# Optimization experiments

Measured on AMD Instinct MI355X. Metric: run time of the kernel, lower is better.

Reference implementation:

```python
import jax, jax.numpy as jnp
import numpy as np

N_NODES = 245760      # 8192 graphs * 30 atoms
N_GRAPHS = 8192
N_EDGES = 1000000
NODES_PER_GRAPH = 30
F_NODE = 78
F_CELL = 1000
HID = 64


def _lin(key, fan_in, fan_out):
    kw, kb = jax.random.split(key)
    s = 1.0 / np.sqrt(fan_in)
    W = jax.random.uniform(kw, (fan_in, fan_out), minval=-s, maxval=s, dtype=jnp.float32)
    b = jax.random.uniform(kb, (fan_out,), minval=-s, maxval=s, dtype=jnp.float32)
    return W, b


def setup_inputs() -> dict:
    key = jax.random.key(0)
    ks = jax.random.split(key, 14)
    x = jax.random.normal(ks[0], (N_NODES, F_NODE), dtype=jnp.float32)
    # edges constrained within each graph: node = graph_id * 30 + local offset
    offs = jax.random.randint(ks[1], (2, N_EDGES), 0, NODES_PER_GRAPH)
    ge = jax.random.randint(ks[2], (N_EDGES,), 0, N_GRAPHS)
    edge_index = (ge[None, :] * NODES_PER_GRAPH + offs).astype(jnp.int64)
    batch = jnp.repeat(jnp.arange(N_GRAPHS, dtype=jnp.int64), NODES_PER_GRAPH)
    cell_features = jax.random.normal(ks[3], (N_GRAPHS, F_CELL), dtype=jnp.float32)
    W1, b1 = _lin(ks[4], F_NODE, HID)
    W2, b2 = _lin(ks[5], HID, 2 * HID)
    W3, b3 = _lin(ks[6], 2 * HID, 4 * HID)
    Wd, bd = _lin(ks[7], 4 * HID, HID)          # drug_embed_fc
    Wc1, bc1 = _lin(ks[8], F_CELL, 2 * HID)      # cell_fc1
    Wc2, bc2 = _lin(ks[9], 2 * HID, HID)         # cell_fc2
    Wm1, bm1 = _lin(ks[10], 2 * HID, HID)        # combiner_fc1
    Wm2, bm2 = _lin(ks[11], HID, 32)             # combiner_fc2
    Wo, bo = _lin(ks[12], 32, 1)                 # output_fc
    return {"x": x, "edge_index": edge_index, "batch": batch,
            "cell_features": cell_features,
            "W1": W1, "b1": b1, "W2": W2, "b2": b2, "W3": W3, "b3": b3,
            "Wd": Wd, "bd": bd, "Wc1": Wc1, "bc1": bc1, "Wc2": Wc2, "bc2": bc2,
            "Wm1": Wm1, "bm1": bm1, "Wm2": Wm2, "bm2": bm2, "Wo": Wo, "bo": bo}


def _gcn_conv(h, W, b, srcA, dstA, norm, n_nodes):
    # PyG GCNConv: linear transform, then sym-normalized scatter-add (self-loops included in srcA/dstA/norm)
    h = h @ W                                   # [N, out]
    msg = h[srcA] * norm[:, None]               # gather + edge scaling
    out = jnp.zeros((n_nodes, W.shape[1]), h.dtype).at[dstA].add(msg)
    return out + b


def reference(x, edge_index, batch, cell_features,
              W1, b1, W2, b2, W3, b3, Wd, bd,
              Wc1, bc1, Wc2, bc2, Wm1, bm1, Wm2, bm2, Wo, bo):
    n = x.shape[0]
    loops = jnp.arange(n, dtype=edge_index.dtype)
    srcA = jnp.concatenate([edge_index[0], loops])
    dstA = jnp.concatenate([edge_index[1], loops])
    deg = jax.ops.segment_sum(jnp.ones_like(dstA, dtype=x.dtype), dstA, num_segments=n)
    dinv = jax.lax.rsqrt(deg)                   # deg >= 1 due to self-loops
    norm = dinv[srcA] * dinv[dstA]

    h = jax.nn.relu(_gcn_conv(x, W1, b1, srcA, dstA, norm, n))
    h = jax.nn.relu(_gcn_conv(h, W2, b2, srcA, dstA, norm, n))
    h = jax.nn.relu(_gcn_conv(h, W3, b3, srcA, dstA, norm, n))

    # global mean pool over graphs
    sums = jax.ops.segment_sum(h, batch, num_segments=N_GRAPHS)
    cnts = jax.ops.segment_sum(jnp.ones((n,), h.dtype), batch, num_segments=N_GRAPHS)
    drug = (sums / cnts[:, None]) @ Wd + bd     # [B, HID]

    cell = jax.nn.relu(cell_features @ Wc1 + bc1)
    cell = cell @ Wc2 + bc2                      # [B, HID]

    comb = jnp.concatenate([drug, cell], axis=1)
    z = jax.nn.relu(comb @ Wm1 + bm1)
    z = jax.nn.relu(z @ Wm2 + bm2)
    out = z @ Wo + bo
    return out.reshape(-1)
```

## Files before the change

### kernel.cpp

```cpp
#include <hip/hip_runtime.h>

typedef __attribute__((ext_vector_type(8))) short short8;
typedef __attribute__((ext_vector_type(4))) short short4v;
typedef __attribute__((ext_vector_type(4))) float f32x4;
typedef unsigned short u16;

__device__ __forceinline__ u16 f2bf(float f) {
    union { float f; unsigned u; } v; v.f = f;
    unsigned r = v.u + 0x7FFFu + ((v.u >> 16) & 1u);
    return (u16)(r >> 16);
}
__device__ __forceinline__ float bf2f(u16 h) {
    union { unsigned u; float f; } v; v.u = ((unsigned)h) << 16;
    return v.f;
}
__device__ __forceinline__ void split2(float f, u16& h, u16& l) {
    h = f2bf(f);
    l = f2bf(f - bf2f(h));
}
__device__ __forceinline__ short8 ld8(const u16* p) {
    short4v a = *(const short4v*)p;
    short4v b = *(const short4v*)(p + 4);
    short8 r;
    r[0] = a[0]; r[1] = a[1]; r[2] = a[2]; r[3] = a[3];
    r[4] = b[0]; r[5] = b[1]; r[6] = b[2]; r[7] = b[3];
    return r;
}
#define MFMA(A, B, C) __builtin_amdgcn_mfma_f32_16x16x32_bf16(A, B, C, 0, 0, 0)

__global__ __launch_bounds__(256) void k_prep(int4* __restrict__ A32z, int nz4,
        const float* __restrict__ W1, u16* __restrict__ W1h, u16* __restrict__ W1l,
        const float* __restrict__ W2, u16* __restrict__ W2h, u16* __restrict__ W2l,
        const float* __restrict__ W3, u16* __restrict__ W3h, u16* __restrict__ W3l,
        const float* __restrict__ Wc1, u16* __restrict__ Wc1h, u16* __restrict__ Wc1l) {
    int i = blockIdx.x * 256 + threadIdx.x;
    if (i < nz4) { A32z[i] = make_int4(0, 0, 0, 0); return; }
    i -= nz4;
    const float* W; u16 *th, *tl; int K, F, Kp;
    if (i < 6144)                        { W = W1;  th = W1h;  tl = W1l;  K = 78;   F = 64;  Kp = 96; }
    else if (i < 6144 + 8192)            { i -= 6144; W = W2;  th = W2h;  tl = W2l;  K = 64;   F = 128; Kp = 64; }
    else if (i < 6144 + 8192 + 32768)    { i -= 6144 + 8192; W = W3;  th = W3h;  tl = W3l;  K = 128;  F = 256; Kp = 128; }
    else if (i < 6144 + 8192 + 32768 + 131072) { i -= 6144 + 8192 + 32768; W = Wc1; th = Wc1h; tl = Wc1l; K = 1000; F = 128; Kp = 1024; }
    else return;
    int f = i / Kp, k = i - f * Kp;
    float v = (k < K) ? W[(size_t)k * F + f] : 0.f;
    u16 h, l; split2(v, h, l);
    th[i] = h; tl[i] = l;
}

__global__ void k_cnt(const int* __restrict__ ei, unsigned* __restrict__ A32, int E) {
    int e = blockIdx.x * 256 + threadIdx.x;
    if (e >= E) return;
    int s = ei[e], d = ei[E + e];
    int g = d / 30;
    int idx = g * 960 + (d - g * 30) * 32 + (s - g * 30);
    atomicAdd(&A32[idx >> 1], 1u << ((idx & 1) * 16));
}

__global__ __launch_bounds__(512, 8) void k_nodecell(
    const float* __restrict__ x, const unsigned* __restrict__ A32,
    const u16* __restrict__ W1h, const u16* __restrict__ W1l,
    const u16* __restrict__ W2h, const u16* __restrict__ W2l,
    const u16* __restrict__ W3h, const u16* __restrict__ W3l,
    const float* __restrict__ b1, const float* __restrict__ b2,
    const float* __restrict__ b3, float* __restrict__ P,
    const float* __restrict__ cf,
    const u16* __restrict__ Wc1h, const u16* __restrict__ Wc1l,
    const float* __restrict__ bc1, float* __restrict__ cell1,
    int CELLB) {
    __shared__ __align__(16) char smem[39936];
    int t = threadIdx.x;
    int wave = t >> 6, lane = t & 63, quad = lane >> 4, l15 = lane & 15;

    if (blockIdx.x < CELLB) {
        u16* Xh = (u16*)(smem + 0);
        u16* Xl = (u16*)(smem + 17920);
        int row0 = blockIdx.x * 64;
        int half = wave >> 2, wq = wave & 3;
        f32x4 acc[2][2] = {{{0.f,0.f,0.f,0.f},{0.f,0.f,0.f,0.f}},
                           {{0.f,0.f,0.f,0.f},{0.f,0.f,0.f,0.f}}};
        for (int ko = 0; ko < 8; ko++) {
#pragma unroll
            for (int ii = 0; ii < 4; ii++) {
                int i = t + ii * 512;
                int r = i >> 5, c4 = i & 31;
                int col = ko * 128 + c4 * 4;
                float4 v = {0.f, 0.f, 0.f, 0.f};
                if (col < 1000) v = *(const float4*)(cf + (size_t)(row0 + r) * 1000 + col);
                float vv[4] = {v.x, v.y, v.z, v.w};
                short4v hs, ls;
#pragma unroll
                for (int j = 0; j < 4; j++) {
                    u16 h, l; split2(vv[j], h, l);
                    hs[j] = (short)h; ls[j] = (short)l;
                }
                *(short4v*)(Xh + r * 140 + c4 * 4) = hs;
                *(short4v*)(Xl + r * 140 + c4 * 4) = ls;
            }
            __syncthreads();
#pragma unroll
            for (int kk = 0; kk < 4; kk++) {
                int klo = kk * 32 + quad * 8;
                short8 ah[2], al[2];
#pragma unroll
                for (int mi = 0; mi < 2; mi++) {
                    ah[mi] = ld8(&Xh[(half * 32 + mi * 16 + l15) * 140 + klo]);
                    al[mi] = ld8(&Xl[(half * 32 + mi * 16 + l15) * 140 + klo]);
                }
#pragma unroll
                for (int ni = 0; ni < 2; ni++) {
                    int col = wq * 32 + ni * 16 + l15;
                    size_t o = (size_t)col * 1024 + ko * 128 + kk * 32 + quad * 8;
                    short8 bh = *(const short8*)(Wc1h + o);
                    short8 bl = *(const short8*)(Wc1l + o);
#pragma unroll
                    for (int mi = 0; mi < 2; mi++) {
                        acc[mi][ni] = MFMA(ah[mi], bh, acc[mi][ni]);
                        acc[mi][ni] = MFMA(al[mi], bh, acc[mi][ni]);
                        acc[mi][ni] = MFMA(ah[mi], bl, acc[mi][ni]);
                    }
                }
            }
            __syncthreads();
        }
#pragma unroll
        for (int ni = 0; ni < 2; ni++) {
            int col = wq * 32 + ni * 16 + l15;
            float bv = bc1[col];
#pragma unroll
            for (int mi = 0; mi < 2; mi++)
#pragma unroll
                for (int rg = 0; rg < 4; rg++) {
                    int row = row0 + half * 32 + mi * 16 + quad * 4 + rg;
                    cell1[(size_t)row * 128 + col] = fmaxf(acc[mi][ni][rg] + bv, 0.f);
                }
        }
        return;
    }

    int g = blockIdx.x - CELLB;
    u16* xh  = (u16*)(smem + 0);
    u16* xl  = (u16*)(smem + 6400);
    u16* h1h = (u16*)(smem + 0);
    u16* h1l = (u16*)(smem + 4352);
    u16* a3h = (u16*)(smem + 0);
    u16* a3l = (u16*)(smem + 8448);
    float* Afp = (float*)(smem + 16896);
    float* dv  = (float*)(smem + 20736);
    u16* t1h = (u16*)(smem + 16896);
    u16* t1l = (u16*)(smem + 21504);
    u16* h2h = (u16*)(smem + 16896);
    u16* h2l = (u16*)(smem + 26112);
    u16* Ah  = (u16*)(smem + 35328);
    u16* Al  = (u16*)(smem + 37632);

    {
        for (int i = t; i < 860; i += 512) {
            uint* arr = (uint*)((i >= 430) ? (char*)xl : (char*)xh);
            int j = (i >= 430) ? i - 430 : i;
            int r, c32;
            if (j < 330) { r = j / 11; c32 = 39 + j % 11; }
            else { r = 30 + (j - 330) / 50; c32 = (j - 330) % 50; }
            arr[r * 50 + c32] = 0;
        }
        const float4* xg = (const float4*)(x + (size_t)g * 2340);
        for (int i = t; i < 585; i += 512) {
            float4 v = xg[i];
            int base = i * 4;
            float vv[4] = {v.x, v.y, v.z, v.w};
#pragma unroll
            for (int j = 0; j < 4; j++) {
                int idx = base + j;
                int r = idx / 78, c = idx - r * 78;
                u16 h, l; split2(vv[j], h, l);
                xh[r * 100 + c] = h; xl[r * 100 + c] = l;
            }
        }
        const unsigned* ac = A32 + (size_t)g * 480;
        for (int i = t; i < 480; i += 512) {
            unsigned w = ac[i];
            Afp[2 * i] = (float)(w & 0xFFFFu);
            Afp[2 * i + 1] = (float)(w >> 16);
        }
        if (t < 32) {
            float s = 1.f;
            if (t < 30) {
                const unsigned* rp = ac + t * 16;
                unsigned acc = 0;
#pragma unroll
                for (int j = 0; j < 16; j++) { unsigned w = rp[j]; acc += (w & 0xFFFFu) + (w >> 16); }
                s += (float)acc;
            }
            dv[t] = (t < 30) ? rsqrtf(s) : 0.f;
        }
    }
    __syncthreads();
    {
#pragma unroll
        for (int ii = 0; ii < 2; ii++) {
            int i = t + ii * 512;
            int r = i >> 5, c = i & 31;
            float a = 0.f;
            if (r < 30 && c < 30)
                a = (Afp[r * 32 + c] + (r == c ? 1.f : 0.f)) * dv[r] * dv[c];
            u16 h, l; split2(a, h, l);
            Ah[r * 36 + c] = h; Al[r * 36 + c] = l;
        }
    }
    __syncthreads();
    {
        int wm = wave >> 2, wn = wave & 3;
        int arow = wm * 16 + l15;
        int col = wn * 16 + l15;
        const u16* wph = W1h + col * 96 + quad * 8;
        const u16* wpl = W1l + col * 96 + quad * 8;
        f32x4 acc = {0.f, 0.f, 0.f, 0.f};
#pragma unroll
        for (int ch = 0; ch < 3; ch++) {
            int kc = ch * 32;
            short8 bh = *(const short8*)(wph + kc);
            short8 bl = *(const short8*)(wpl + kc);
            short8 ah = ld8(&xh[arow * 100 + kc + quad * 8]);
            short8 al = ld8(&xl[arow * 100 + kc + quad * 8]);
            acc = MFMA(ah, bh, acc);
            acc = MFMA(al, bh, acc);
            acc = MFMA(ah, bl, acc);
        }
#pragma unroll
        for (int rg = 0; rg < 4; rg++) {
            int row = wm * 16 + quad * 4 + rg;
            u16 h, l; split2(acc[rg], h, l);
            t1h[col * 36 + row] = h;
            t1l[col * 36 + row] = l;
        }
    }
    __syncthreads();
    {
        int wm = wave >> 2, wn = wave & 3;
        int arow = wm * 16 + l15;
        int col = wn * 16 + l15;
        short8 aAh = ld8(&Ah[arow * 36 + quad * 8]);
        short8 aAl = ld8(&Al[arow * 36 + quad * 8]);
        short8 bh = ld8(&t1h[col * 36 + quad * 8]);
        short8 bl = ld8(&t1l[col * 36 + quad * 8]);
        f32x4 acc = {0.f, 0.f, 0.f, 0.f};
        acc = MFMA(aAh, bh, acc);
        acc = MFMA(aAl, bh, acc);
        acc = MFMA(aAh, bl, acc);
        float bb = b1[col];
#pragma unroll
        for (int rg = 0; rg < 4; rg++) {
            int row = wm * 16 + quad * 4 + rg;
            float v = fmaxf(acc[rg] + bb, 0.f);
            u16 h, l; split2(v, h, l);
            h1h[row * 68 + col] = h;
            h1l[row * 68 + col] = l;
        }
    }
    __syncthreads();
    {
        int col = wave * 16 + l15;
        const u16* wph = W2h + col * 64 + quad * 8;
        const u16* wpl = W2l + col * 64 + quad * 8;
        f32x4 acc[2] = {{0.f,0.f,0.f,0.f},{0.f,0.f,0.f,0.f}};
#pragma unroll
        for (int ch = 0; ch < 2; ch++) {
            int kc = ch * 32;
            short8 bh = *(const short8*)(wph + kc);
            short8 bl = *(const short8*)(wpl + kc);
#pragma unroll
            for (int mi = 0; mi < 2; mi++) {
                short8 ah = ld8(&h1h[(mi * 16 + l15) * 68 + kc + quad * 8]);
                short8 al = ld8(&h1l[(mi * 16 + l15) * 68 + kc + quad * 8]);
                acc[mi] = MFMA(ah, bh, acc[mi]);
                acc[mi] = MFMA(al, bh, acc[mi]);
                acc[mi] = MFMA(ah, bl, acc[mi]);
            }
        }
        float bb = b2[col];
#pragma unroll
        for (int mi = 0; mi < 2; mi++)
#pragma unroll
            for (int rg = 0; rg < 4; rg++) {
                int row = mi * 16 + quad * 4 + rg;
                float v = fmaxf(acc[mi][rg] + bb, 0.f);
                u16 h, l; split2(v, h, l);
                h2h[col * 36 + row] = h;
                h2l[col * 36 + row] = l;
            }
    }
    __syncthreads();
    {
        int col = wave * 16 + l15;
        short8 bh = ld8(&h2h[col * 36 + quad * 8]);
        short8 bl = ld8(&h2l[col * 36 + quad * 8]);
        f32x4 acc[2] = {{0.f,0.f,0.f,0.f},{0.f,0.f,0.f,0.f}};
#pragma unroll
        for (int mi = 0; mi < 2; mi++) {
            short8 aAh = ld8(&Ah[(mi * 16 + l15) * 36 + quad * 8]);
            short8 aAl = ld8(&Al[(mi * 16 + l15) * 36 + quad * 8]);
            acc[mi] = MFMA(aAh, bh, acc[mi]);
            acc[mi] = MFMA(aAl, bh, acc[mi]);
            acc[mi] = MFMA(aAh, bl, acc[mi]);
        }
#pragma unroll
        for (int mi = 0; mi < 2; mi++)
#pragma unroll
            for (int rg = 0; rg < 4; rg++) {
                int row = mi * 16 + quad * 4 + rg;
                u16 h, l; split2(acc[mi][rg], h, l);
                a3h[row * 132 + col] = h;
                a3l[row * 132 + col] = l;
            }
    }
    __syncthreads();
    {
        int colb = wave * 32;
        f32x4 acc[2][2] = {{{0.f,0.f,0.f,0.f},{0.f,0.f,0.f,0.f}},
                           {{0.f,0.f,0.f,0.f},{0.f,0.f,0.f,0.f}}};
        short8 cwh[2], cwl[2], nwh[2], nwl[2];
#pragma unroll
        for (int ni = 0; ni < 2; ni++) {
            size_t o = (size_t)(colb + ni * 16 + l15) * 128 + quad * 8;
            cwh[ni] = *(const short8*)(W3h + o);
            cwl[ni] = *(const short8*)(W3l + o);
        }
#pragma unroll
        for (int ch = 0; ch < 4; ch++) {
            if (ch < 3) {
#pragma unroll
                for (int ni = 0; ni < 2; ni++) {
                    size_t o = (size_t)(colb + ni * 16 + l15) * 128 + (ch + 1) * 32 + quad * 8;
                    nwh[ni] = *(const short8*)(W3h + o);
                    nwl[ni] = *(const short8*)(W3l + o);
                }
            }
            short8 ah[2], al[2];
#pragma unroll
            for (int mi = 0; mi < 2; mi++) {
                ah[mi] = ld8(&a3h[(mi * 16 + l15) * 132 + ch * 32 + quad * 8]);
                al[mi] = ld8(&a3l[(mi * 16 + l15) * 132 + ch * 32 + quad * 8]);
            }
#pragma unroll
            for (int mi = 0; mi < 2; mi++)
#pragma unroll
                for (int ni = 0; ni < 2; ni++) {
                    acc[mi][ni] = MFMA(ah[mi], cwh[ni], acc[mi][ni]);
                    acc[mi][ni] = MFMA(al[mi], cwh[ni], acc[mi][ni]);
                    acc[mi][ni] = MFMA(ah[mi], cwl[ni], acc[mi][ni]);
                }
            if (ch < 3) {
#pragma unroll
                for (int ni = 0; ni < 2; ni++) { cwh[ni] = nwh[ni]; cwl[ni] = nwl[ni]; }
            }
        }
#pragma unroll
        for (int ni = 0; ni < 2; ni++) {
            int col = colb + ni * 16 + l15;
            float bb = b3[col];
            float p = 0.f;
#pragma unroll
            for (int mi = 0; mi < 2; mi++)
#pragma unroll
                for (int rg = 0; rg < 4; rg++) {
                    int row = mi * 16 + quad * 4 + rg;
                    if (row < 30) p += fmaxf(acc[mi][ni][rg] + bb, 0.f);
                }
            p += __shfl_down(p, 32);
            p += __shfl_down(p, 16);
            if (lane < 16)
                P[(size_t)g * 256 + colb + ni * 16 + lane] = p * (1.0f / 30.0f);
        }
    }
}

__global__ __launch_bounds__(256) void k_tail(const float* __restrict__ pooled,
        const float* __restrict__ cell1,
        const float* __restrict__ Wd, const float* __restrict__ bd,
        const float* __restrict__ Wc2, const float* __restrict__ bc2,
        const float* __restrict__ Wm1, const float* __restrict__ bm1,
        const float* __restrict__ Wm2, const float* __restrict__ bm2,
        const float* __restrict__ Wo, const float* __restrict__ bo,
        float* __restrict__ out) {
    __shared__ float pr[1024];
    __shared__ float c1[512];
    __shared__ float dz[512];
    __shared__ float z1f[256];
    __shared__ float z2f[128];
    int t = threadIdx.x;
    int g0 = blockIdx.x * 4;
    int gl = t >> 6, c = t & 63;
    ((float4*)pr)[t] = ((const float4*)(pooled + (size_t)g0 * 256))[t];
    if (t < 128) ((float4*)c1)[t] = ((const float4*)(cell1 + (size_t)g0 * 128))[t];
    __syncthreads();
    float s = bd[c];
#pragma unroll 8
    for (int k = 0; k < 256; k++) s += pr[gl * 256 + k] * Wd[k * 64 + c];
    dz[gl * 128 + c] = s;
    float s2 = bc2[c];
#pragma unroll 8
    for (int k = 0; k < 128; k++) s2 += c1[gl * 128 + k] * Wc2[k * 64 + c];
    dz[gl * 128 + 64 + c] = s2;
    __syncthreads();
    float s3 = bm1[c];
#pragma unroll 8
    for (int k = 0; k < 128; k++) s3 += dz[gl * 128 + k] * Wm1[k * 64 + c];
    z1f[gl * 64 + c] = fmaxf(s3, 0.f);
    __syncthreads();
    if (c < 32) {
        float s4 = bm2[c];
#pragma unroll 8
        for (int k = 0; k < 64; k++) s4 += z1f[gl * 64 + k] * Wm2[k * 32 + c];
        z2f[gl * 32 + c] = fmaxf(s4, 0.f);
    }
    __syncthreads();
    float v = (c < 32) ? z2f[gl * 32 + c] * Wo[c] : 0.f;
#pragma unroll
    for (int off = 32; off > 0; off >>= 1) v += __shfl_down(v, off);
    if (c == 0) out[g0 + gl] = v + bo[0];
}


extern "C" void kernel_launch(void* const* d_in, const int* in_sizes, int n_in,
                              void* d_out, int out_size, void* d_ws, size_t ws_size,
                              hipStream_t stream) {
    const float* x   = (const float*)d_in[0];
    const int*   ei  = (const int*)d_in[1];
    const float* cf  = (const float*)d_in[3];
    const float* W1  = (const float*)d_in[4];
    const float* b1  = (const float*)d_in[5];
    const float* W2  = (const float*)d_in[6];
    const float* b2  = (const float*)d_in[7];
    const float* W3  = (const float*)d_in[8];
    const float* b3  = (const float*)d_in[9];
    const float* Wd  = (const float*)d_in[10];
    const float* bd  = (const float*)d_in[11];
    const float* Wc1 = (const float*)d_in[12];
    const float* bc1 = (const float*)d_in[13];
    const float* Wc2 = (const float*)d_in[14];
    const float* bc2 = (const float*)d_in[15];
    const float* Wm1 = (const float*)d_in[16];
    const float* bm1 = (const float*)d_in[17];
    const float* Wm2 = (const float*)d_in[18];
    const float* bm2 = (const float*)d_in[19];
    const float* Wo  = (const float*)d_in[20];
    const float* bo  = (const float*)d_in[21];
    float* out = (float*)d_out;

    const int E = in_sizes[1] / 2;
    const int B = in_sizes[3] / 1000;

    char* w = (char*)d_ws;
    auto carve = [&](size_t bytes) { void* p = (void*)w; w += (bytes + 255) & ~(size_t)255; return p; };
    unsigned* A32 = (unsigned*)carve((size_t)B * 960 * 2);
    float* pooled = (float*)carve((size_t)B * 256 * 4);
    float* cell1  = (float*)carve((size_t)B * 128 * 4);
    u16* W1th = (u16*)carve(64 * 96 * 2);     u16* W1tl = (u16*)carve(64 * 96 * 2);
    u16* W2th = (u16*)carve(128 * 64 * 2);    u16* W2tl = (u16*)carve(128 * 64 * 2);
    u16* W3th = (u16*)carve(256 * 128 * 2);   u16* W3tl = (u16*)carve(256 * 128 * 2);
    u16* Wc1th = (u16*)carve(128 * 1024 * 2); u16* Wc1tl = (u16*)carve(128 * 1024 * 2);

    auto g1 = [](int n) { return (n + 255) / 256; };

    const int nz4 = B * 120;
    const int nsplit = 6144 + 8192 + 32768 + 131072;

    k_prep<<<g1(nz4 + nsplit), 256, 0, stream>>>((int4*)A32, nz4,
        W1, W1th, W1tl, W2, W2th, W2tl, W3, W3th, W3tl, Wc1, Wc1th, Wc1tl);

    k_cnt<<<g1(E), 256, 0, stream>>>(ei, A32, E);

    const int CELLB = B / 64;
    k_nodecell<<<CELLB + B, 512, 0, stream>>>(x, A32,
                                  W1th, W1tl, W2th, W2tl, W3th, W3tl,
                                  b1, b2, b3, pooled,
                                  cf, Wc1th, Wc1tl, bc1, cell1, CELLB);

    k_tail<<<B / 4, 256, 0, stream>>>(pooled, cell1, Wd, bd, Wc2, bc2,
                                      Wm1, bm1, Wm2, bm2, Wo, bo, out);
}
```

Before: 445.8 us.

## Bucket edges per 8-graph group, build adjacency histogram in shared memory

Replaces the global per-edge atomic increments into the dense per-graph adjacency count array with a two-pass scheme. First each edge is appended as a packed 16-bit code into a per-bucket list (8 graphs per bucket) using one atomic per edge on a small counter array. Then one block per bucket builds the histogram with shared-memory atomics and writes it out with coalesced vector stores. This also removes the need to zero the full adjacency array beforehand. The trade-off is an extra kernel launch and a fixed bucket capacity (BCAP), so edges beyond it are silently dropped if a bucket overflows.

```diff
diff --git a/kernel.cpp b/kernel.cpp
--- a/kernel.cpp
+++ b/kernel.cpp
@@ -4,6 +4,8 @@
 typedef __attribute__((ext_vector_type(4))) short short4v;
 typedef __attribute__((ext_vector_type(4))) float f32x4;
 typedef unsigned short u16;
+
+#define BCAP 1536
 
 __device__ __forceinline__ u16 f2bf(float f) {
     union { float f; unsigned u; } v; v.f = f;
@@ -28,14 +30,14 @@
 }
 #define MFMA(A, B, C) __builtin_amdgcn_mfma_f32_16x16x32_bf16(A, B, C, 0, 0, 0)
 
-__global__ __launch_bounds__(256) void k_prep(int4* __restrict__ A32z, int nz4,
+__global__ __launch_bounds__(256) void k_prep(int4* __restrict__ bcnt4,
         const float* __restrict__ W1, u16* __restrict__ W1h, u16* __restrict__ W1l,
         const float* __restrict__ W2, u16* __restrict__ W2h, u16* __restrict__ W2l,
         const float* __restrict__ W3, u16* __restrict__ W3h, u16* __restrict__ W3l,
         const float* __restrict__ Wc1, u16* __restrict__ Wc1h, u16* __restrict__ Wc1l) {
     int i = blockIdx.x * 256 + threadIdx.x;
-    if (i < nz4) { A32z[i] = make_int4(0, 0, 0, 0); return; }
-    i -= nz4;
+    if (i < 256) { bcnt4[i] = make_int4(0, 0, 0, 0); return; }
+    i -= 256;
     const float* W; u16 *th, *tl; int K, F, Kp;
     if (i < 6144)                        { W = W1;  th = W1h;  tl = W1l;  K = 78;   F = 64;  Kp = 96; }
     else if (i < 6144 + 8192)            { i -= 6144; W = W2;  th = W2h;  tl = W2l;  K = 64;   F = 128; Kp = 64; }
@@ -48,13 +50,36 @@
     th[i] = h; tl[i] = l;
 }
 
-__global__ void k_cnt(const int* __restrict__ ei, unsigned* __restrict__ A32, int E) {
+__global__ void k_bkt(const int* __restrict__ ei, unsigned* __restrict__ bcnt,
+                      u16* __restrict__ bedge, int E) {
     int e = blockIdx.x * 256 + threadIdx.x;
     if (e >= E) return;
     int s = ei[e], d = ei[E + e];
     int g = d / 30;
-    int idx = g * 960 + (d - g * 30) * 32 + (s - g * 30);
-    atomicAdd(&A32[idx >> 1], 1u << ((idx & 1) * 16));
+    int b = g >> 3;
+    unsigned code = ((unsigned)(g & 7) << 10) | ((unsigned)(d - g * 30) << 5)
+                  | (unsigned)(s - g * 30);
+    unsigned slot = atomicAdd(&bcnt[b], 1u);
+    if (slot < BCAP) bedge[(size_t)b * BCAP + slot] = (u16)code;
+}
+
+__global__ __launch_bounds__(256) void k_hist(const unsigned* __restrict__ bcnt,
+        const u16* __restrict__ bedge, unsigned* __restrict__ A32) {
+    __shared__ __align__(16) unsigned h[3840];
+    int t = threadIdx.x, b = blockIdx.x;
+    for (int i = t; i < 3840; i += 256) h[i] = 0;
+    __syncthreads();
+    int n = bcnt[b]; if (n > BCAP) n = BCAP;
+    const u16* be = bedge + (size_t)b * BCAP;
+    for (int i = t; i < n; i += 256) {
+        unsigned c = be[i];
+        unsigned idx = (c >> 10) * 960 + ((c >> 5) & 31) * 32 + (c & 31);
+        atomicAdd(&h[idx >> 1], 1u << ((idx & 1) * 16));
+    }
+    __syncthreads();
+    int4* dst = (int4*)(A32 + (size_t)b * 3840);
+    const int4* src = (const int4*)h;
+    for (int i = t; i < 960; i += 256) dst[i] = src[i];
 }
 
 __global__ __launch_bounds__(512, 8) void k_nodecell(
@@ -449,6 +474,7 @@
 
     const int E = in_sizes[1] / 2;
     const int B = in_sizes[3] / 1000;
+    const int NBKT = B / 8;
 
     char* w = (char*)d_ws;
     auto carve = [&](size_t bytes) { void* p = (void*)w; w += (bytes + 255) & ~(size_t)255; return p; };
@@ -459,16 +485,19 @@
     u16* W2th = (u16*)carve(128 * 64 * 2);    u16* W2tl = (u16*)carve(128 * 64 * 2);
     u16* W3th = (u16*)carve(256 * 128 * 2);   u16* W3tl = (u16*)carve(256 * 128 * 2);
     u16* Wc1th = (u16*)carve(128 * 1024 * 2); u16* Wc1tl = (u16*)carve(128 * 1024 * 2);
+    unsigned* bcnt = (unsigned*)carve((size_t)NBKT * 4);
+    u16* bedge = (u16*)carve((size_t)NBKT * BCAP * 2);
 
     auto g1 = [](int n) { return (n + 255) / 256; };
 
-    const int nz4 = B * 120;
     const int nsplit = 6144 + 8192 + 32768 + 131072;
 
-    k_prep<<<g1(nz4 + nsplit), 256, 0, stream>>>((int4*)A32, nz4,
+    k_prep<<<g1(256 + nsplit), 256, 0, stream>>>((int4*)bcnt,
         W1, W1th, W1tl, W2, W2th, W2tl, W3, W3th, W3tl, Wc1, Wc1th, Wc1tl);
 
-    k_cnt<<<g1(E), 256, 0, stream>>>(ei, A32, E);
+    k_bkt<<<g1(E), 256, 0, stream>>>(ei, bcnt, bedge, E);
+
+    k_hist<<<NBKT, 256, 0, stream>>>(bcnt, bedge, A32);
 
     const int CELLB = B / 64;
     k_nodecell<<<CELLB + B, 512, 0, stream>>>(x, A32,
```

Result: slower. 611.5 us (+37.2%).

## Build adjacency counts with per-block LDS histograms instead of global atomics

Applied to the files above, without the earlier changes.

Edges are first encoded into compact 32-bit codes (graph, dst, src). Each block of 32 graphs then scans the full code array, accumulating packed 16-bit counts in shared memory with LDS atomics, and writes its slice of the count matrix directly. This removes the separate zeroing of the count buffer and the global atomics. In exchange, every block rereads all edge codes, so total read traffic grows with the number of blocks.

```diff
diff --git a/kernel.cpp b/kernel.cpp
--- a/kernel.cpp
+++ b/kernel.cpp
@@ -28,14 +28,12 @@
 }
 #define MFMA(A, B, C) __builtin_amdgcn_mfma_f32_16x16x32_bf16(A, B, C, 0, 0, 0)
 
-__global__ __launch_bounds__(256) void k_prep(int4* __restrict__ A32z, int nz4,
+__global__ __launch_bounds__(256) void k_prep(
         const float* __restrict__ W1, u16* __restrict__ W1h, u16* __restrict__ W1l,
         const float* __restrict__ W2, u16* __restrict__ W2h, u16* __restrict__ W2l,
         const float* __restrict__ W3, u16* __restrict__ W3h, u16* __restrict__ W3l,
         const float* __restrict__ Wc1, u16* __restrict__ Wc1h, u16* __restrict__ Wc1l) {
     int i = blockIdx.x * 256 + threadIdx.x;
-    if (i < nz4) { A32z[i] = make_int4(0, 0, 0, 0); return; }
-    i -= nz4;
     const float* W; u16 *th, *tl; int K, F, Kp;
     if (i < 6144)                        { W = W1;  th = W1h;  tl = W1l;  K = 78;   F = 64;  Kp = 96; }
     else if (i < 6144 + 8192)            { i -= 6144; W = W2;  th = W2h;  tl = W2l;  K = 64;   F = 128; Kp = 64; }
@@ -48,13 +46,48 @@
     th[i] = h; tl[i] = l;
 }
 
-__global__ void k_cnt(const int* __restrict__ ei, unsigned* __restrict__ A32, int E) {
+__global__ void k_code(const int* __restrict__ ei, unsigned* __restrict__ code, int E) {
     int e = blockIdx.x * 256 + threadIdx.x;
     if (e >= E) return;
     int s = ei[e], d = ei[E + e];
     int g = d / 30;
-    int idx = g * 960 + (d - g * 30) * 32 + (s - g * 30);
-    atomicAdd(&A32[idx >> 1], 1u << ((idx & 1) * 16));
+    code[e] = ((unsigned)g << 10) | ((unsigned)(d - g * 30) << 5) | (unsigned)(s - g * 30);
+}
+
+#define GPB 32
+__global__ __launch_bounds__(512) void k_hist(const unsigned* __restrict__ code,
+        unsigned* __restrict__ A32, int E) {
+    __shared__ __align__(16) unsigned h[GPB * 480];
+    int t = threadIdx.x, b = blockIdx.x;
+    unsigned glo = (unsigned)b * GPB;
+    for (int i = t; i < GPB * 480; i += 512) h[i] = 0;
+    __syncthreads();
+    const int4* c4 = (const int4*)code;
+    int n4 = E >> 2;
+    for (int i = t; i < n4; i += 512) {
+        int4 v = c4[i];
+        unsigned cs[4] = {(unsigned)v.x, (unsigned)v.y, (unsigned)v.z, (unsigned)v.w};
+#pragma unroll
+        for (int j = 0; j < 4; j++) {
+            unsigned rg = (cs[j] >> 10) - glo;
+            if (rg < GPB) {
+                unsigned idx = rg * 960 + (cs[j] & 1023u);
+                atomicAdd(&h[idx >> 1], 1u << ((idx & 1) * 16));
+            }
+        }
+    }
+    if (t < (E & 3)) {
+        unsigned c = code[(E & ~3) + t];
+        unsigned rg = (c >> 10) - glo;
+        if (rg < GPB) {
+            unsigned idx = rg * 960 + (c & 1023u);
+            atomicAdd(&h[idx >> 1], 1u << ((idx & 1) * 16));
+        }
+    }
+    __syncthreads();
+    int4* dst = (int4*)(A32 + (size_t)b * GPB * 480);
+    const int4* src = (const int4*)h;
+    for (int i = t; i < GPB * 120; i += 512) dst[i] = src[i];
 }
 
 __global__ __launch_bounds__(512, 8) void k_nodecell(
@@ -459,16 +492,18 @@
     u16* W2th = (u16*)carve(128 * 64 * 2);    u16* W2tl = (u16*)carve(128 * 64 * 2);
     u16* W3th = (u16*)carve(256 * 128 * 2);   u16* W3tl = (u16*)carve(256 * 128 * 2);
     u16* Wc1th = (u16*)carve(128 * 1024 * 2); u16* Wc1tl = (u16*)carve(128 * 1024 * 2);
+    unsigned* code = (unsigned*)carve((size_t)E * 4);
 
     auto g1 = [](int n) { return (n + 255) / 256; };
 
-    const int nz4 = B * 120;
     const int nsplit = 6144 + 8192 + 32768 + 131072;
 
-    k_prep<<<g1(nz4 + nsplit), 256, 0, stream>>>((int4*)A32, nz4,
+    k_code<<<g1(E), 256, 0, stream>>>(ei, code, E);
+
+    k_prep<<<g1(nsplit), 256, 0, stream>>>(
         W1, W1th, W1tl, W2, W2th, W2tl, W3, W3th, W3tl, Wc1, Wc1th, Wc1tl);
 
-    k_cnt<<<g1(E), 256, 0, stream>>>(ei, A32, E);
+    k_hist<<<B / GPB, 512, 0, stream>>>(code, A32, E);
 
     const int CELLB = B / 64;
     k_nodecell<<<CELLB + B, 512, 0, stream>>>(x, A32,
```

After: 588.8 us. +32.1%, slower.

## Run the tail MLP on bf16x3 MFMA with 32 graphs per block

Applied to the files above, without the earlier changes.

Replaces the scalar FP32 tail MLP (drug/cell projections, combiner layers, output) with a matrix-core version that uses split bf16 hi/lo operands (three MFMAs per product) and processes 32 graphs per block instead of 4. The tail weights are pre-split and transposed in the existing prep kernel. This removes scalar FMA loops that reread the weights from global memory for every few graphs. In exchange it adds split/convert work and shared-memory staging. The tail is a small share of total time, so the overall gain is bounded.

```diff
diff --git a/kernel.cpp b/kernel.cpp
--- a/kernel.cpp
+++ b/kernel.cpp
@@ -32,15 +32,23 @@
         const float* __restrict__ W1, u16* __restrict__ W1h, u16* __restrict__ W1l,
         const float* __restrict__ W2, u16* __restrict__ W2h, u16* __restrict__ W2l,
         const float* __restrict__ W3, u16* __restrict__ W3h, u16* __restrict__ W3l,
-        const float* __restrict__ Wc1, u16* __restrict__ Wc1h, u16* __restrict__ Wc1l) {
+        const float* __restrict__ Wc1, u16* __restrict__ Wc1h, u16* __restrict__ Wc1l,
+        const float* __restrict__ Wd, u16* __restrict__ WdTh, u16* __restrict__ WdTl,
+        const float* __restrict__ Wc2, u16* __restrict__ Wc2Th, u16* __restrict__ Wc2Tl,
+        const float* __restrict__ Wm1, u16* __restrict__ Wm1Th, u16* __restrict__ Wm1Tl,
+        const float* __restrict__ Wm2, u16* __restrict__ Wm2Th, u16* __restrict__ Wm2Tl) {
     int i = blockIdx.x * 256 + threadIdx.x;
     if (i < nz4) { A32z[i] = make_int4(0, 0, 0, 0); return; }
     i -= nz4;
     const float* W; u16 *th, *tl; int K, F, Kp;
-    if (i < 6144)                        { W = W1;  th = W1h;  tl = W1l;  K = 78;   F = 64;  Kp = 96; }
-    else if (i < 6144 + 8192)            { i -= 6144; W = W2;  th = W2h;  tl = W2l;  K = 64;   F = 128; Kp = 64; }
-    else if (i < 6144 + 8192 + 32768)    { i -= 6144 + 8192; W = W3;  th = W3h;  tl = W3l;  K = 128;  F = 256; Kp = 128; }
-    else if (i < 6144 + 8192 + 32768 + 131072) { i -= 6144 + 8192 + 32768; W = Wc1; th = Wc1h; tl = Wc1l; K = 1000; F = 128; Kp = 1024; }
+    if (i < 6144)        { W = W1;  th = W1h;  tl = W1l;  K = 78;   F = 64;  Kp = 96; }
+    else if (i < 14336)  { i -= 6144;   W = W2;  th = W2h;  tl = W2l;  K = 64;   F = 128; Kp = 64; }
+    else if (i < 47104)  { i -= 14336;  W = W3;  th = W3h;  tl = W3l;  K = 128;  F = 256; Kp = 128; }
+    else if (i < 178176) { i -= 47104;  W = Wc1; th = Wc1h; tl = Wc1l; K = 1000; F = 128; Kp = 1024; }
+    else if (i < 194560) { i -= 178176; W = Wd;  th = WdTh; tl = WdTl; K = 256;  F = 64;  Kp = 256; }
+    else if (i < 202752) { i -= 194560; W = Wc2; th = Wc2Th; tl = Wc2Tl; K = 128; F = 64; Kp = 128; }
+    else if (i < 210944) { i -= 202752; W = Wm1; th = Wm1Th; tl = Wm1Tl; K = 128; F = 64; Kp = 128; }
+    else if (i < 212992) { i -= 210944; W = Wm2; th = Wm2Th; tl = Wm2Tl; K = 64;  F = 32; Kp = 64; }
     else return;
     int f = i / Kp, k = i - f * Kp;
     float v = (k < K) ? W[(size_t)k * F + f] : 0.f;
@@ -374,50 +382,157 @@
     }
 }
 
-__global__ __launch_bounds__(256) void k_tail(const float* __restrict__ pooled,
+__global__ __launch_bounds__(256) void k_tail2(const float* __restrict__ pooled,
         const float* __restrict__ cell1,
-        const float* __restrict__ Wd, const float* __restrict__ bd,
-        const float* __restrict__ Wc2, const float* __restrict__ bc2,
-        const float* __restrict__ Wm1, const float* __restrict__ bm1,
-        const float* __restrict__ Wm2, const float* __restrict__ bm2,
+        const u16* __restrict__ WdTh, const u16* __restrict__ WdTl, const float* __restrict__ bd,
+        const u16* __restrict__ Wc2Th, const u16* __restrict__ Wc2Tl, const float* __restrict__ bc2,
+        const u16* __restrict__ Wm1Th, const u16* __restrict__ Wm1Tl, const float* __restrict__ bm1,
+        const u16* __restrict__ Wm2Th, const u16* __restrict__ Wm2Tl, const float* __restrict__ bm2,
         const float* __restrict__ Wo, const float* __restrict__ bo,
         float* __restrict__ out) {
-    __shared__ float pr[1024];
-    __shared__ float c1[512];
-    __shared__ float dz[512];
-    __shared__ float z1f[256];
-    __shared__ float z2f[128];
+    __shared__ __align__(16) char smem[50176];
+    u16* Xh  = (u16*)(smem);
+    u16* Xl  = (u16*)(smem + 25088);
+    u16* dzh = (u16*)(smem);
+    u16* dzl = (u16*)(smem + 8960);
+    u16* z1h = (u16*)(smem + 17920);
+    u16* z1l = (u16*)(smem + 22528);
+    float* z2f = (float*)(smem + 27136);
     int t = threadIdx.x;
-    int g0 = blockIdx.x * 4;
-    int gl = t >> 6, c = t & 63;
-    ((float4*)pr)[t] = ((const float4*)(pooled + (size_t)g0 * 256))[t];
-    if (t < 128) ((float4*)c1)[t] = ((const float4*)(cell1 + (size_t)g0 * 128))[t];
-    __syncthreads();
-    float s = bd[c];
+    int row0 = blockIdx.x * 32;
+    int wave = t >> 6, lane = t & 63, quad = lane >> 4, l15 = lane & 15;
+
+#pragma unroll
+    for (int ii = 0; ii < 12; ii++) {
+        int i = t + ii * 256;
+        int r = i / 96, c4 = i - r * 96;
+        float4 v = (c4 < 64)
+            ? ((const float4*)(pooled + (size_t)(row0 + r) * 256))[c4]
+            : ((const float4*)(cell1 + (size_t)(row0 + r) * 128))[c4 - 64];
+        float vv[4] = {v.x, v.y, v.z, v.w};
+        short4v hs, ls;
+#pragma unroll
+        for (int j = 0; j < 4; j++) {
+            u16 h, l; split2(vv[j], h, l);
+            hs[j] = (short)h; ls[j] = (short)l;
+        }
+        *(short4v*)(Xh + r * 392 + c4 * 4) = hs;
+        *(short4v*)(Xl + r * 392 + c4 * 4) = ls;
+    }
+    __syncthreads();
+
+    bool cw = wave >= 2;
+    int nbase = (wave & 1) * 32;
+    const u16* Bh = cw ? Wc2Th : WdTh;
+    const u16* Bl = cw ? Wc2Tl : WdTl;
+    const int Kp = cw ? 128 : 256;
+    const int nch = cw ? 4 : 8;
+    const int acol = cw ? 256 : 0;
+    f32x4 acc[2][2] = {{{0.f,0.f,0.f,0.f},{0.f,0.f,0.f,0.f}},
+                       {{0.f,0.f,0.f,0.f},{0.f,0.f,0.f,0.f}}};
+    for (int ch = 0; ch < nch; ch++) {
+        int kc = ch * 32 + quad * 8;
+        short8 ah[2], al[2];
+#pragma unroll
+        for (int mi = 0; mi < 2; mi++) {
+            ah[mi] = ld8(&Xh[(mi * 16 + l15) * 392 + acol + kc]);
+            al[mi] = ld8(&Xl[(mi * 16 + l15) * 392 + acol + kc]);
+        }
+#pragma unroll
+        for (int ni = 0; ni < 2; ni++) {
+            int col = nbase + ni * 16 + l15;
+            short8 bh = *(const short8*)(Bh + (size_t)col * Kp + kc);
+            short8 bl = *(const short8*)(Bl + (size_t)col * Kp + kc);
+#pragma unroll
+            for (int mi = 0; mi < 2; mi++) {
+                acc[mi][ni] = MFMA(ah[mi], bh, acc[mi][ni]);
+                acc[mi][ni] = MFMA(al[mi], bh, acc[mi][ni]);
+                acc[mi][ni] = MFMA(ah[mi], bl, acc[mi][ni]);
+            }
+        }
+    }
+    __syncthreads();
+#pragma unroll
+    for (int ni = 0; ni < 2; ni++) {
+        int c = nbase + ni * 16 + l15;
+        float bb = cw ? bc2[c] : bd[c];
+        int col = (cw ? 64 : 0) + c;
+#pragma unroll
+        for (int mi = 0; mi < 2; mi++)
+#pragma unroll
+            for (int rg = 0; rg < 4; rg++) {
+                int row = mi * 16 + quad * 4 + rg;
+                u16 h, l; split2(acc[mi][ni][rg] + bb, h, l);
+                dzh[row * 140 + col] = h;
+                dzl[row * 140 + col] = l;
+            }
+    }
+    __syncthreads();
+
+    {
+        int col = wave * 16 + l15;
+        f32x4 a2[2] = {{0.f,0.f,0.f,0.f},{0.f,0.f,0.f,0.f}};
+#pragma unroll
+        for (int ch = 0; ch < 4; ch++) {
+            int kc = ch * 32 + quad * 8;
+            short8 bh = *(const short8*)(Wm1Th + (size_t)col * 128 + kc);
+            short8 bl = *(const short8*)(Wm1Tl + (size_t)col * 128 + kc);
+#pragma unroll
+            for (int mi = 0; mi < 2; mi++) {
+                short8 ah = ld8(&dzh[(mi * 16 + l15) * 140 + kc]);
+                short8 al = ld8(&dzl[(mi * 16 + l15) * 140 + kc]);
+                a2[mi] = MFMA(ah, bh, a2[mi]);
+                a2[mi] = MFMA(al, bh, a2[mi]);
+                a2[mi] = MFMA(ah, bl, a2[mi]);
+            }
+        }
+        float bb = bm1[col];
+#pragma unroll
+        for (int mi = 0; mi < 2; mi++)
+#pragma unroll
+            for (int rg = 0; rg < 4; rg++) {
+                int row = mi * 16 + quad * 4 + rg;
+                u16 h, l; split2(fmaxf(a2[mi][rg] + bb, 0.f), h, l);
+                z1h[row * 72 + col] = h;
+                z1l[row * 72 + col] = l;
+            }
+    }
+    __syncthreads();
+
+    if (wave < 2) {
+        int col = wave * 16 + l15;
+        f32x4 a3[2] = {{0.f,0.f,0.f,0.f},{0.f,0.f,0.f,0.f}};
+#pragma unroll
+        for (int ch = 0; ch < 2; ch++) {
+            int kc = ch * 32 + quad * 8;
+            short8 bh = *(const short8*)(Wm2Th + (size_t)col * 64 + kc);
+            short8 bl = *(const short8*)(Wm2Tl + (size_t)col * 64 + kc);
+#pragma unroll
+            for (int mi = 0; mi < 2; mi++) {
+                short8 ah = ld8(&z1h[(mi * 16 + l15) * 72 + kc]);
+                short8 al = ld8(&z1l[(mi * 16 + l15) * 72 + kc]);
+                a3[mi] = MFMA(ah, bh, a3[mi]);
+                a3[mi] = MFMA(al, bh, a3[mi]);
+                a3[mi] = MFMA(ah, bl, a3[mi]);
+            }
+        }
+        float bb = bm2[col];
+#pragma unroll
+        for (int mi = 0; mi < 2; mi++)
+#pragma unroll
+            for (int rg = 0; rg < 4; rg++) {
+                int row = mi * 16 + quad * 4 + rg;
+                z2f[row * 33 + col] = fmaxf(a3[mi][rg] + bb, 0.f);
+            }
+    }
+    __syncthreads();
+
+    if (t < 32) {
+        float s = bo[0];
 #pragma unroll 8
-    for (int k = 0; k < 256; k++) s += pr[gl * 256 + k] * Wd[k * 64 + c];
-    dz[gl * 128 + c] = s;
-    float s2 = bc2[c];
-#pragma unroll 8
-    for (int k = 0; k < 128; k++) s2 += c1[gl * 128 + k] * Wc2[k * 64 + c];
-    dz[gl * 128 + 64 + c] = s2;
-    __syncthreads();
-    float s3 = bm1[c];
-#pragma unroll 8
-    for (int k = 0; k < 128; k++) s3 += dz[gl * 128 + k] * Wm1[k * 64 + c];
-    z1f[gl * 64 + c] = fmaxf(s3, 0.f);
-    __syncthreads();
-    if (c < 32) {
-        float s4 = bm2[c];
-#pragma unroll 8
-        for (int k = 0; k < 64; k++) s4 += z1f[gl * 64 + k] * Wm2[k * 32 + c];
-        z2f[gl * 32 + c] = fmaxf(s4, 0.f);
-    }
-    __syncthreads();
-    float v = (c < 32) ? z2f[gl * 32 + c] * Wo[c] : 0.f;
-#pragma unroll
-    for (int off = 32; off > 0; off >>= 1) v += __shfl_down(v, off);
-    if (c == 0) out[g0 + gl] = v + bo[0];
+        for (int k = 0; k < 32; k++) s += z2f[t * 33 + k] * Wo[k];
+        out[row0 + t] = s;
+    }
 }
 
 
@@ -459,14 +574,19 @@
     u16* W2th = (u16*)carve(128 * 64 * 2);    u16* W2tl = (u16*)carve(128 * 64 * 2);
     u16* W3th = (u16*)carve(256 * 128 * 2);   u16* W3tl = (u16*)carve(256 * 128 * 2);
     u16* Wc1th = (u16*)carve(128 * 1024 * 2); u16* Wc1tl = (u16*)carve(128 * 1024 * 2);
+    u16* WdTh = (u16*)carve(64 * 256 * 2);    u16* WdTl = (u16*)carve(64 * 256 * 2);
+    u16* Wc2Th = (u16*)carve(64 * 128 * 2);   u16* Wc2Tl = (u16*)carve(64 * 128 * 2);
+    u16* Wm1Th = (u16*)carve(64 * 128 * 2);   u16* Wm1Tl = (u16*)carve(64 * 128 * 2);
+    u16* Wm2Th = (u16*)carve(32 * 64 * 2);    u16* Wm2Tl = (u16*)carve(32 * 64 * 2);
 
     auto g1 = [](int n) { return (n + 255) / 256; };
 
     const int nz4 = B * 120;
-    const int nsplit = 6144 + 8192 + 32768 + 131072;
+    const int nsplit = 212992;
 
     k_prep<<<g1(nz4 + nsplit), 256, 0, stream>>>((int4*)A32, nz4,
-        W1, W1th, W1tl, W2, W2th, W2tl, W3, W3th, W3tl, Wc1, Wc1th, Wc1tl);
+        W1, W1th, W1tl, W2, W2th, W2tl, W3, W3th, W3tl, Wc1, Wc1th, Wc1tl,
+        Wd, WdTh, WdTl, Wc2, Wc2Th, Wc2Tl, Wm1, Wm1Th, Wm1Tl, Wm2, Wm2Th, Wm2Tl);
 
     k_cnt<<<g1(E), 256, 0, stream>>>(ei, A32, E);
 
@@ -476,6 +596,8 @@
                                   b1, b2, b3, pooled,
                                   cf, Wc1th, Wc1tl, bc1, cell1, CELLB);
 
-    k_tail<<<B / 4, 256, 0, stream>>>(pooled, cell1, Wd, bd, Wc2, bc2,
-                                      Wm1, bm1, Wm2, bm2, Wo, bo, out);
-}
+    k_tail2<<<B / 32, 256, 0, stream>>>(pooled, cell1,
+                                        WdTh, WdTl, bd, Wc2Th, Wc2Tl, bc2,
+                                        Wm1Th, Wm1Tl, bm1, Wm2Th, Wm2Tl, bm2,
+                                        Wo, bo, out);
+}
```

New measurement: 419.0 us. -6.0%, faster.
